# Kernel optimization log

Measured on AMD Instinct MI355X. Metric: run time of the kernel, lower is better.

## Reference

```python
import jax, jax.numpy as jnp
import numpy as np

DIM = 32          # d_model == channel dim of the volume
D_STATE = 16
D_CONV = 4
EXPAND = 2
D_INNER = EXPAND * DIM        # 64
DT_RANK = max(1, (DIM + 15) // 16)  # ceil(d_model/16) = 2
LN_EPS = 1e-5


def setup_inputs() -> dict:
    key = jax.random.key(0)
    ks = jax.random.split(key, 12)
    B, Dd, Hh, Ww = 1, 32, 32, 32
    sc = 0.02
    x = jax.random.normal(ks[0], (B, DIM, Dd, Hh, Ww), jnp.float32)
    ln_w = jnp.ones((DIM,), jnp.float32)
    ln_b = jnp.zeros((DIM,), jnp.float32)
    in_proj_w = jax.random.normal(ks[1], (2 * D_INNER, DIM), jnp.float32) * sc
    conv_w = jax.random.normal(ks[2], (D_INNER, 1, D_CONV), jnp.float32) * sc
    conv_b = jnp.zeros((D_INNER,), jnp.float32)
    x_proj_w = jax.random.normal(ks[3], (DT_RANK + 2 * D_STATE, D_INNER), jnp.float32) * sc
    dt_proj_w = jax.random.normal(ks[4], (D_INNER, DT_RANK), jnp.float32) * sc
    dt_proj_b = jax.random.uniform(ks[5], (D_INNER,), jnp.float32, -4.0, -2.0)  # small softplus(dt) at init
    # Mamba S4D-real init: A = -[1..d_state], stored as A_log
    A_log = jnp.log(jnp.broadcast_to(jnp.arange(1, D_STATE + 1, dtype=jnp.float32), (D_INNER, D_STATE)))
    D_param = jnp.ones((D_INNER,), jnp.float32)
    out_proj_w = jax.random.normal(ks[6], (DIM, D_INNER), jnp.float32) * sc
    return {
        "x": x, "ln_w": ln_w, "ln_b": ln_b, "in_proj_w": in_proj_w,
        "conv_w": conv_w, "conv_b": conv_b, "x_proj_w": x_proj_w,
        "dt_proj_w": dt_proj_w, "dt_proj_b": dt_proj_b, "A_log": A_log,
        "D_param": D_param, "out_proj_w": out_proj_w,
    }


def _mamba_layer(x, ln_w, ln_b, in_proj_w, conv_w, conv_b, x_proj_w,
                 dt_proj_w, dt_proj_b, A_log, D_param, out_proj_w):
    B, C, Dd, Hh, Ww = x.shape
    L = Dd * Hh * Ww
    # z-scan flatten: (B, C, D, H, W) -> (B, L, C)
    xf = x.reshape(B, C, L).transpose(0, 2, 1)
    # LayerNorm over channel dim
    mu = jnp.mean(xf, axis=-1, keepdims=True)
    var = jnp.mean(jnp.square(xf - mu), axis=-1, keepdims=True)
    xn = (xf - mu) * jax.lax.rsqrt(var + LN_EPS) * ln_w + ln_b
    # in_proj -> x, z branches
    xz = xn @ in_proj_w.T                      # (B, L, 2*d_inner)
    x_in, z = jnp.split(xz, 2, axis=-1)
    # depthwise causal conv1d over sequence
    xt = x_in.transpose(0, 2, 1)               # (B, d_inner, L)
    xc = jax.lax.conv_general_dilated(
        xt, conv_w, window_strides=(1,), padding=[(D_CONV - 1, 0)],
        feature_group_count=D_INNER)
    xc = jax.nn.silu(xc + conv_b[None, :, None]).transpose(0, 2, 1)  # (B, L, d_inner)
    # input-dependent dt, B, C
    x_dbl = xc @ x_proj_w.T                    # (B, L, dt_rank + 2*d_state)
    dt, Bm, Cm = jnp.split(x_dbl, [DT_RANK, DT_RANK + D_STATE], axis=-1)
    delta = jax.nn.softplus(dt @ dt_proj_w.T + dt_proj_b)            # (B, L, d_inner)
    A = -jnp.exp(A_log)                        # (d_inner, d_state)
    # discretize: h_t = exp(delta*A) h_{t-1} + delta*B_t*x_t
    dA = jnp.exp(delta[..., None] * A)                               # (B, L, d_inner, d_state)
    dBx = delta[..., None] * Bm[:, :, None, :] * xc[..., None]       # (B, L, d_inner, d_state)
    def comb(e1, e2):
        a1, b1 = e1
        a2, b2 = e2
        return (a1 * a2, a2 * b1 + b2)
    _, h = jax.lax.associative_scan(comb, (dA, dBx), axis=1)         # parallel linear recurrence
    y = jnp.einsum('blds,bls->bld', h, Cm) + xc * D_param            # (B, L, d_inner)
    y = y * jax.nn.silu(z)
    out = y @ out_proj_w.T                     # (B, L, C)
    # unpermute z-scan
    return out.transpose(0, 2, 1).reshape(B, C, Dd, Hh, Ww)


def reference(x, ln_w, ln_b, in_proj_w, conv_w, conv_b, x_proj_w,
              dt_proj_w, dt_proj_b, A_log, D_param, out_proj_w):
    return _mamba_layer(x, ln_w, ln_b, in_proj_w, conv_w, conv_b, x_proj_w,
                        dt_proj_w, dt_proj_b, A_log, D_param, out_proj_w)
```

## Files before the change

kernel.cpp:

```cpp
#include <hip/hip_runtime.h>
#include <hip/hip_bf16.h>

constexpr int L   = 32768;
constexpr int CD  = 32;
constexpr int DI  = 64;
constexpr int DS  = 16;
constexpr int LC  = 32;
constexpr int NCH = L / LC;
constexpr int NPAIR = DI * DS;

constexpr size_t FL        = (size_t)DI * L;
constexpr size_t OFF_XC    = 0;
constexpr size_t OFF_DELTA = FL;
constexpr size_t OFF_BM    = 2 * FL;
constexpr size_t OFF_CM    = OFF_BM + (size_t)DS * L;
constexpr size_t OFF_APROD = OFF_CM + (size_t)DS * L;
constexpr size_t OFF_CARRY = OFF_APROD;
constexpr size_t OFF_BACC  = OFF_APROD + (size_t)NCH * NPAIR;

__device__ __forceinline__ float bf2f(__hip_bfloat16 v) { return __bfloat162float(v); }

__device__ __forceinline__ bool detect_bf16(const void* ln_w) {
    return ((const unsigned short*)ln_w)[0] == 0x3F80;
}
__device__ __forceinline__ float ldin(const void* p, size_t i, bool bf16) {
    return bf16 ? bf2f(((const __hip_bfloat16*)p)[i]) : ((const float*)p)[i];
}

__device__ __forceinline__ float dot32_g(const void* w, int row, const float* xv, bool isb) {
    float acc = 0.f;
    if (isb) {
        const __hip_bfloat16* p = (const __hip_bfloat16*)w + (size_t)row * 32;
        #pragma unroll
        for (int c = 0; c < 32; ++c) acc += bf2f(p[c]) * xv[c];
    } else {
        const float4* p = (const float4*)((const float*)w + (size_t)row * 32);
        #pragma unroll
        for (int q = 0; q < 8; ++q) {
            const float4 w4 = p[q];
            acc += w4.x * xv[4*q] + w4.y * xv[4*q+1] + w4.z * xv[4*q+2] + w4.w * xv[4*q+3];
        }
    }
    return acc;
}

__global__ __launch_bounds__(256, 2) void k12_featurize_scan(
    const void* __restrict__ x,
    const void* __restrict__ ln_w,
    const void* __restrict__ ln_b,
    const void* __restrict__ in_proj_w,
    const void* __restrict__ conv_w,
    const void* __restrict__ conv_b,
    const void* __restrict__ x_proj_w,
    const void* __restrict__ dt_proj_w,
    const void* __restrict__ dt_proj_b,
    const void* __restrict__ A_log,
    float* __restrict__ ws)
{
    __shared__ __align__(16) char smem[33808];
    float (*xin_s)[37]  = (float(*)[37])(smem);
    float (*sxc)[36]    = (float(*)[36])(smem);
    char* AR = smem + 9472;
    float (*xn_s)[33]   = (float(*)[33])(AR);
    float (*w_in_s)[32] = (float(*)[32])(AR + 4624);
    float (*sdl)[36]    = (float(*)[36])(AR);
    float (*sbm)[36]    = (float(*)[36])(AR + 9216);
    char* FW = smem + 22288;
    float (*w_xp)[64]   = (float(*)[64])(FW);
    float (*w_cv)[5]    = (float(*)[5])(FW + 8704);
    float (*w_dt)[3]    = (float(*)[3])(FW + 9984);
    float* b_dt_s = (float*)(FW + 10752);
    float* b_cv_s = (float*)(FW + 11008);
    float* lnw_s  = (float*)(FW + 11264);
    float* lnb_s  = (float*)(FW + 11392);

    const int tid = threadIdx.x;
    const int l0  = blockIdx.x * LC;
    const bool isb = detect_bf16(ln_w);

    if (isb) {
        const __hip_bfloat16* ipw = (const __hip_bfloat16*)in_proj_w;
        const __hip_bfloat16* xpw = (const __hip_bfloat16*)x_proj_w;
        for (int i = tid; i < 64 * 32; i += 256) ((float*)w_in_s)[i] = bf2f(ipw[i]);
        for (int i = tid; i < 34 * 64; i += 256) ((float*)w_xp)[i] = bf2f(xpw[i]);
    } else {
        const float4* ipw = (const float4*)in_proj_w;
        const float4* xpw = (const float4*)x_proj_w;
        #pragma unroll
        for (int k = 0; k < 2; ++k) ((float4*)w_in_s)[tid + 256 * k] = ipw[tid + 256 * k];
        for (int i = tid; i < 544; i += 256) ((float4*)w_xp)[i] = xpw[i];
    }
    w_cv[tid >> 2][tid & 3] = ldin(conv_w, tid, isb);
    if (tid < 128) w_dt[tid >> 1][tid & 1] = ldin(dt_proj_w, tid, isb);
    if (tid < 64) { b_dt_s[tid] = ldin(dt_proj_b, tid, isb); b_cv_s[tid] = ldin(conv_b, tid, isb); }
    if (tid < 32) { lnw_s[tid] = ldin(ln_w, tid, isb); lnb_s[tid] = ldin(ln_b, tid, isb); }
    __syncthreads();

    if (tid < 140) {
        const int pos = tid >> 2;
        const int q   = tid & 3;
        const int l = l0 - 3 + pos;
        const bool valid = (l >= 0);
        const int lc = valid ? l : 0;
        float xq[8];
        #pragma unroll
        for (int i = 0; i < 8; ++i) xq[i] = ldin(x, (size_t)(q * 8 + i) * L + lc, isb);
        float s = 0.f;
        #pragma unroll
        for (int i = 0; i < 8; ++i) s += xq[i];
        s += __shfl_xor(s, 1);
        s += __shfl_xor(s, 2);
        const float mu = s * (1.f / CD);
        float d2 = 0.f;
        #pragma unroll
        for (int i = 0; i < 8; ++i) { const float dc = xq[i] - mu; d2 += dc * dc; }
        d2 += __shfl_xor(d2, 1);
        d2 += __shfl_xor(d2, 2);
        const float rstd = rsqrtf(d2 * (1.f / CD) + 1e-5f);
        #pragma unroll
        for (int i = 0; i < 8; ++i) {
            const int ch = q * 8 + i;
            xn_s[pos][ch] = valid ? ((xq[i] - mu) * rstd * lnw_s[ch] + lnb_s[ch]) : 0.f;
        }
    }
    __syncthreads();

    {
        const int colq = tid & 31;
        const int rgrp = tid >> 5;
        float xv[CD];
        #pragma unroll
        for (int c = 0; c < CD; ++c) xv[c] = xn_s[colq][c];
        #pragma unroll 2
        for (int j = 0; j < 8; ++j) {
            const int row = rgrp * 8 + j;
            const float4* wr = (const float4*)w_in_s[row];
            float a0 = 0.f;
            #pragma unroll
            for (int q = 0; q < 8; ++q) {
                const float4 w4 = wr[q];
                a0 += w4.x * xv[4*q] + w4.y * xv[4*q+1] + w4.z * xv[4*q+2] + w4.w * xv[4*q+3];
            }
            xin_s[row][colq] = a0;
        }
        if (tid < 192) {
            const int row = tid & 63;
            const int cH  = 32 + (tid >> 6);
            float xvh[CD];
            #pragma unroll
            for (int c = 0; c < CD; ++c) xvh[c] = xn_s[cH][c];
            xin_s[row][cH] = dot32_g(in_proj_w, row, xvh, isb);
        }
    }
    __syncthreads();

    {
        const int h  = tid & 7;
        const int pq = tid >> 3;
        const int l  = l0 + pq;
        const int dbase = h * 8;
        float xcv[8];
        #pragma unroll
        for (int i = 0; i < 8; ++i) {
            const int d = dbase + i;
            float acc = b_cv_s[d];
            #pragma unroll
            for (int k = 0; k < 4; ++k) acc += w_cv[d][k] * xin_s[d][pq + k];
            const float v = acc / (1.f + __expf(-acc));
            xcv[i] = v;
            ws[OFF_XC + (size_t)d * L + l] = v;
        }
        float dt0 = 0.f, dt1 = 0.f;
        for (int r = 0; r < 34; ++r) {
            const float4 wa = *(const float4*)&w_xp[r][dbase];
            const float4 wb = *(const float4*)&w_xp[r][dbase + 4];
            float acc = wa.x * xcv[0] + wa.y * xcv[1] + wa.z * xcv[2] + wa.w * xcv[3]
                      + wb.x * xcv[4] + wb.y * xcv[5] + wb.z * xcv[6] + wb.w * xcv[7];
            acc += __shfl_xor(acc, 1);
            acc += __shfl_xor(acc, 2);
            acc += __shfl_xor(acc, 4);
            if (r == 0) dt0 = acc;
            else if (r == 1) dt1 = acc;
            else {
                const int rr = r - 2;
                if (h == (rr >> 2)) {
                    const size_t off = (rr < 16) ? (OFF_BM + (size_t)rr * L)
                                                 : (OFF_CM + (size_t)(rr - 16) * L);
                    ws[off + l] = acc;
                    if (rr < 16) sbm[rr][pq] = acc;
                }
            }
        }
        #pragma unroll
        for (int i = 0; i < 8; ++i) {
            const int d = dbase + i;
            const float tv = dt0 * w_dt[d][0] + dt1 * w_dt[d][1] + b_dt_s[d];
            const float sp = fmaxf(tv, 0.f) + log1pf(__expf(-fabsf(tv)));
            ws[OFF_DELTA + (size_t)d * L + l] = sp;
            sdl[d][pq] = sp;
        }
        __syncthreads();
        #pragma unroll
        for (int i = 0; i < 8; ++i) sxc[dbase + i][pq] = xcv[i];
    }
    __syncthreads();

    {
        const int d = tid >> 2, sg = tid & 3;
        float Aj[4], ap[4] = {1.f, 1.f, 1.f, 1.f}, bb[4] = {0.f, 0.f, 0.f, 0.f};
        #pragma unroll
        for (int j = 0; j < 4; ++j) Aj[j] = -__expf(ldin(A_log, d * DS + sg + 4 * j, isb));

        auto cstep = [&](float dd, float xx, float m0, float m1, float m2, float m3) {
            const float dxc = dd * xx;
            float e;
            e = __expf(dd * Aj[0]); ap[0] *= e; bb[0] = e * bb[0] + dxc * m0;
            e = __expf(dd * Aj[1]); ap[1] *= e; bb[1] = e * bb[1] + dxc * m1;
            e = __expf(dd * Aj[2]); ap[2] *= e; bb[2] = e * bb[2] + dxc * m2;
            e = __expf(dd * Aj[3]); ap[3] *= e; bb[3] = e * bb[3] + dxc * m3;
        };
        for (int t = 0; t < LC; t += 4) {
            const float4 dd4 = *(const float4*)&sdl[d][t];
            const float4 xx4 = *(const float4*)&sxc[d][t];
            const float4 b0 = *(const float4*)&sbm[sg][t];
            const float4 b1 = *(const float4*)&sbm[sg + 4][t];
            const float4 b2 = *(const float4*)&sbm[sg + 8][t];
            const float4 b3 = *(const float4*)&sbm[sg + 12][t];
            cstep(dd4.x, xx4.x, b0.x, b1.x, b2.x, b3.x);
            cstep(dd4.y, xx4.y, b0.y, b1.y, b2.y, b3.y);
            cstep(dd4.z, xx4.z, b0.z, b1.z, b2.z, b3.z);
            cstep(dd4.w, xx4.w, b0.w, b1.w, b2.w, b3.w);
        }
        *(float4*)&ws[OFF_APROD + (size_t)blockIdx.x * NPAIR + tid * 4] = make_float4(ap[0], ap[1], ap[2], ap[3]);
        *(float4*)&ws[OFF_BACC  + (size_t)blockIdx.x * NPAIR + tid * 4] = make_float4(bb[0], bb[1], bb[2], bb[3]);
    }
}

__global__ __launch_bounds__(256) void k3_carry(float* __restrict__ ws)
{
    __shared__ float ctile[4][NCH];
    const int lane = threadIdx.x & 63;
    const int wv   = threadIdx.x >> 6;
    const int bid  = blockIdx.x;
    const int pg   = ((bid & 7) << 5) | (bid >> 3);
    const int p    = pg * 4 + wv;

    float a[16], b[16];
    #pragma unroll
    for (int i = 0; i < 16; ++i) {
        const size_t ch = (size_t)(lane * 16 + i);
        a[i] = ws[OFF_APROD + ch * NPAIR + p];
        b[i] = ws[OFF_BACC  + ch * NPAIR + p];
    }

    float Ag = a[0], Bg = b[0];
    #pragma unroll
    for (int i = 1; i < 16; ++i) { Bg = a[i] * Bg + b[i]; Ag = Ag * a[i]; }
    #pragma unroll
    for (int off = 1; off < 64; off <<= 1) {
        const float pa = __shfl_up(Ag, off);
        const float pb = __shfl_up(Bg, off);
        if (lane >= off) { Bg = Ag * pb + Bg; Ag = Ag * pa; }
    }
    float Pb = __shfl_up(Bg, 1);
    if (lane == 0) Pb = 0.f;
    #pragma unroll
    for (int i = 0; i < 16; ++i) { ctile[wv][lane * 16 + i] = Pb; Pb = a[i] * Pb + b[i]; }
    __syncthreads();
    #pragma unroll
    for (int r = 0; r < 4; ++r) {
        const int ch = threadIdx.x + 256 * r;
        *(float4*)&ws[OFF_CARRY + (size_t)ch * NPAIR + pg * 4] =
            make_float4(ctile[0][ch], ctile[1][ch], ctile[2][ch], ctile[3][ch]);
    }
}

__global__ __launch_bounds__(256, 2) void k45_apply_out(
    const void* __restrict__ x,
    const void* __restrict__ ln_w,
    const void* __restrict__ ln_b,
    const void* __restrict__ in_proj_w,
    const void* __restrict__ A_log,
    const void* __restrict__ D_param,
    const void* __restrict__ out_proj_w,
    float* __restrict__ ws,
    void* __restrict__ out)
{
    __shared__ __align__(16) char smem45[35712];
    float (*sx)[36]      = (float(*)[36])(smem45);
    float (*sy)[36]      = (float(*)[36])(smem45 + 4608);
    float (*sbm)[36]     = (float(*)[36])(smem45 + 13824);
    float (*scm)[36]     = (float(*)[36])(smem45 + 16128);
    float (*w_z)[33]     = (float(*)[33])(smem45 + 18432);
    float (*w_out_s)[65] = (float(*)[65])(smem45 + 26880);
    float* lnw_s = (float*)(smem45 + 35200);
    float* lnb_s = (float*)(smem45 + 35328);
    float* mu_s  = (float*)(smem45 + 35456);
    float* rs_s  = (float*)(smem45 + 35584);

    const int tid = threadIdx.x;
    const int c   = blockIdx.x;
    const size_t t0 = (size_t)c * LC;
    const bool isb = detect_bf16(ln_w);

    {
        const int r = tid >> 3, t4 = (tid & 7) * 4;
        if (isb) {
            const __hip_bfloat16* xb = (const __hip_bfloat16*)x;
            #pragma unroll
            for (int k = 0; k < 4; ++k) sx[r][t4 + k] = bf2f(xb[(size_t)r * L + t0 + t4 + k]);
        } else {
            *(float4*)&sx[r][t4] = *(const float4*)&((const float*)x)[(size_t)r * L + t0 + t4];
        }
    }
    {
        const int q = tid & 127;
        const int r = q >> 3, t4 = (q & 7) * 4;
        const size_t src = ((tid < 128) ? OFF_BM : OFF_CM) + (size_t)r * L + t0 + t4;
        float* dst = (tid < 128) ? &sbm[r][t4] : &scm[r][t4];
        *(float4*)dst = *(const float4*)&ws[src];
    }
    #pragma unroll
    for (int k = 0; k < 8; ++k) {
        const int idx = tid + 256 * k;
        w_z[idx >> 5][idx & 31] = ldin(in_proj_w, (size_t)(64 << 5) + idx, isb);
    }
    #pragma unroll
    for (int k = 0; k < 8; ++k) {
        const int idx = tid + 256 * k;
        w_out_s[idx >> 6][idx & 63] = ldin(out_proj_w, idx, isb);
    }
    if (tid < 32) { lnw_s[tid] = ldin(ln_w, tid, isb); lnb_s[tid] = ldin(ln_b, tid, isb); }
    __syncthreads();

    if (tid < 128) {
        const int pos = tid >> 2;
        const int q   = tid & 3;
        float s = 0.f;
        #pragma unroll
        for (int i = 0; i < 8; ++i) s += sx[q * 8 + i][pos];
        s += __shfl_xor(s, 1);
        s += __shfl_xor(s, 2);
        const float mu = s * (1.f / CD);
        float d2 = 0.f;
        #pragma unroll
        for (int i = 0; i < 8; ++i) { const float dc = sx[q * 8 + i][pos] - mu; d2 += dc * dc; }
        d2 += __shfl_xor(d2, 1);
        d2 += __shfl_xor(d2, 2);
        if (q == 0) { mu_s[pos] = mu; rs_s[pos] = rsqrtf(d2 * (1.f / CD) + 1e-5f); }
    }
    __syncthreads();

    {
        const int pos  = tid & 31;
        const int rgrp = tid >> 5;
        const float mu = mu_s[pos], rstd = rs_s[pos];
        float acc[8] = {0.f, 0.f, 0.f, 0.f, 0.f, 0.f, 0.f, 0.f};
        for (int ch = 0; ch < CD; ++ch) {
            const float xnc = (sx[ch][pos] - mu) * rstd * lnw_s[ch] + lnb_s[ch];
            #pragma unroll
            for (int j = 0; j < 8; ++j) acc[j] += xnc * w_z[rgrp * 8 + j][ch];
        }
        #pragma unroll
        for (int j = 0; j < 8; ++j)
            sy[rgrp * 8 + j][pos] = acc[j] / (1.f + __expf(-acc[j]));
    }
    __syncthreads();

    {
        const int d = tid >> 2, sg = tid & 3;
        float Aj[4];
        #pragma unroll
        for (int j = 0; j < 4; ++j) Aj[j] = -__expf(ldin(A_log, d * DS + sg + 4 * j, isb));
        const float Dd = ldin(D_param, d, isb);
        float hh[4];
        {
            const float4 h4 = *(const float4*)&ws[OFF_CARRY + (size_t)c * NPAIR + tid * 4];
            hh[0] = h4.x; hh[1] = h4.y; hh[2] = h4.z; hh[3] = h4.w;
        }
        const float* dlp = ws + OFF_DELTA + (size_t)d * L + t0;
        const float* xcp = ws + OFF_XC    + (size_t)d * L + t0;

        auto step = [&](float dd, float xx, int col,
                        float m0, float m1, float m2, float m3,
                        float c0, float c1, float c2, float c3) {
            const float dxc = dd * xx;
            float e, ys;
            e = __expf(dd * Aj[0]); hh[0] = e * hh[0] + dxc * m0; ys  = hh[0] * c0;
            e = __expf(dd * Aj[1]); hh[1] = e * hh[1] + dxc * m1; ys += hh[1] * c1;
            e = __expf(dd * Aj[2]); hh[2] = e * hh[2] + dxc * m2; ys += hh[2] * c2;
            e = __expf(dd * Aj[3]); hh[3] = e * hh[3] + dxc * m3; ys += hh[3] * c3;
            ys += __shfl_xor(ys, 1);
            ys += __shfl_xor(ys, 2);
            if (sg == 0) sy[d][col] *= (ys + xx * Dd);
        };
        for (int t = 0; t < LC; t += 4) {
            const float4 dd4 = *(const float4*)(dlp + t);
            const float4 xx4 = *(const float4*)(xcp + t);
            const float4 b0 = *(const float4*)&sbm[sg][t];
            const float4 b1 = *(const float4*)&sbm[sg + 4][t];
            const float4 b2 = *(const float4*)&sbm[sg + 8][t];
            const float4 b3 = *(const float4*)&sbm[sg + 12][t];
            const float4 c0 = *(const float4*)&scm[sg][t];
            const float4 c1 = *(const float4*)&scm[sg + 4][t];
            const float4 c2 = *(const float4*)&scm[sg + 8][t];
            const float4 c3 = *(const float4*)&scm[sg + 12][t];
            step(dd4.x, xx4.x, t,     b0.x, b1.x, b2.x, b3.x, c0.x, c1.x, c2.x, c3.x);
            step(dd4.y, xx4.y, t + 1, b0.y, b1.y, b2.y, b3.y, c0.y, c1.y, c2.y, c3.y);
            step(dd4.z, xx4.z, t + 2, b0.z, b1.z, b2.z, b3.z, c0.z, c1.z, c2.z, c3.z);
            step(dd4.w, xx4.w, t + 3, b0.w, b1.w, b2.w, b3.w, c0.w, c1.w, c2.w, c3.w);
        }
    }
    __syncthreads();

    {
        const int wv   = tid >> 6;
        const int lane = tid & 63;
        const int pos  = lane & 31;
        const int cg   = lane >> 5;
        const int c0   = wv * 8 + cg * 4;
        float acc[4] = {0.f, 0.f, 0.f, 0.f};
        for (int dd = 0; dd < DI; ++dd) {
            const float yv = sy[dd][pos];
            #pragma unroll
            for (int j = 0; j < 4; ++j)
                acc[j] += yv * w_out_s[c0 + j][dd];
        }
        const size_t l = t0 + pos;
        #pragma unroll
        for (int j = 0; j < 4; ++j) {
            const int cc = c0 + j;
            if (isb) ((__hip_bfloat16*)out)[(size_t)cc * L + l] = __float2bfloat16(acc[j]);
            else     ((float*)out)[(size_t)cc * L + l] = acc[j];
        }
    }
}

extern "C" void kernel_launch(void* const* d_in, const int* in_sizes, int n_in,
                              void* d_out, int out_size, void* d_ws, size_t ws_size,
                              hipStream_t stream)
{
    (void)in_sizes; (void)n_in; (void)out_size; (void)ws_size;
    const void* x        = d_in[0];
    const void* ln_w     = d_in[1];
    const void* ln_b     = d_in[2];
    const void* in_pw    = d_in[3];
    const void* conv_w   = d_in[4];
    const void* conv_b   = d_in[5];
    const void* x_pw     = d_in[6];
    const void* dt_pw    = d_in[7];
    const void* dt_pb    = d_in[8];
    const void* A_log    = d_in[9];
    const void* D_param  = d_in[10];
    const void* out_pw   = d_in[11];
    float* ws = (float*)d_ws;

    k12_featurize_scan<<<NCH, 256, 0, stream>>>(x, ln_w, ln_b, in_pw, conv_w, conv_b,
                                                x_pw, dt_pw, dt_pb, A_log, ws);
    k3_carry<<<NPAIR / 4, 256, 0, stream>>>(ws);
    k45_apply_out<<<NCH, 256, 0, stream>>>(x, ln_w, ln_b, in_pw, A_log, D_param,
                                           out_pw, ws, d_out);
}
```

Baseline: 163.1 us.

## Store workspace intermediates in chunk-tiled layout with coalesced float4 writes

Changes the workspace layout for xc, delta, B and C from feature-major over the full sequence to per-chunk contiguous tiles. The featurize kernel now stages C in shared memory as well and writes all tiles with vectorized float4 stores after a barrier, instead of scattered per-element strided stores. The consumer kernel reads the same data as contiguous tiles. This adds a little shared memory and a copy-out phase in exchange for coalesced global traffic.

```diff
diff --git a/kernel.cpp b/kernel.cpp
--- a/kernel.cpp
+++ b/kernel.cpp
@@ -9,12 +9,11 @@
 constexpr int NCH = L / LC;
 constexpr int NPAIR = DI * DS;
 
-constexpr size_t FL        = (size_t)DI * L;
 constexpr size_t OFF_XC    = 0;
-constexpr size_t OFF_DELTA = FL;
-constexpr size_t OFF_BM    = 2 * FL;
-constexpr size_t OFF_CM    = OFF_BM + (size_t)DS * L;
-constexpr size_t OFF_APROD = OFF_CM + (size_t)DS * L;
+constexpr size_t OFF_DELTA = (size_t)NCH * DI * LC;
+constexpr size_t OFF_BM    = 2 * (size_t)NCH * DI * LC;
+constexpr size_t OFF_CM    = OFF_BM + (size_t)NCH * DS * LC;
+constexpr size_t OFF_APROD = OFF_CM + (size_t)NCH * DS * LC;
 constexpr size_t OFF_CARRY = OFF_APROD;
 constexpr size_t OFF_BACC  = OFF_APROD + (size_t)NCH * NPAIR;
 
@@ -57,7 +56,7 @@
     const void* __restrict__ A_log,
     float* __restrict__ ws)
 {
-    __shared__ __align__(16) char smem[33808];
+    __shared__ __align__(16) char smem[34816];
     float (*xin_s)[37]  = (float(*)[37])(smem);
     float (*sxc)[36]    = (float(*)[36])(smem);
     char* AR = smem + 9472;
@@ -65,7 +64,8 @@
     float (*w_in_s)[32] = (float(*)[32])(AR + 4624);
     float (*sdl)[36]    = (float(*)[36])(AR);
     float (*sbm)[36]    = (float(*)[36])(AR + 9216);
-    char* FW = smem + 22288;
+    float (*scm)[36]    = (float(*)[36])(AR + 11520);
+    char* FW = smem + 23296;
     float (*w_xp)[64]   = (float(*)[64])(FW);
     float (*w_cv)[5]    = (float(*)[5])(FW + 8704);
     float (*w_dt)[3]    = (float(*)[3])(FW + 9984);
@@ -157,7 +157,6 @@
     {
         const int h  = tid & 7;
         const int pq = tid >> 3;
-        const int l  = l0 + pq;
         const int dbase = h * 8;
         float xcv[8];
         #pragma unroll
@@ -166,9 +165,7 @@
             float acc = b_cv_s[d];
             #pragma unroll
             for (int k = 0; k < 4; ++k) acc += w_cv[d][k] * xin_s[d][pq + k];
-            const float v = acc / (1.f + __expf(-acc));
-            xcv[i] = v;
-            ws[OFF_XC + (size_t)d * L + l] = v;
+            xcv[i] = acc / (1.f + __expf(-acc));
         }
         float dt0 = 0.f, dt1 = 0.f;
         for (int r = 0; r < 34; ++r) {
@@ -184,10 +181,8 @@
             else {
                 const int rr = r - 2;
                 if (h == (rr >> 2)) {
-                    const size_t off = (rr < 16) ? (OFF_BM + (size_t)rr * L)
-                                                 : (OFF_CM + (size_t)(rr - 16) * L);
-                    ws[off + l] = acc;
                     if (rr < 16) sbm[rr][pq] = acc;
+                    else         scm[rr - 16][pq] = acc;
                 }
             }
         }
@@ -195,15 +190,29 @@
         for (int i = 0; i < 8; ++i) {
             const int d = dbase + i;
             const float tv = dt0 * w_dt[d][0] + dt1 * w_dt[d][1] + b_dt_s[d];
-            const float sp = fmaxf(tv, 0.f) + log1pf(__expf(-fabsf(tv)));
-            ws[OFF_DELTA + (size_t)d * L + l] = sp;
-            sdl[d][pq] = sp;
+            sdl[d][pq] = fmaxf(tv, 0.f) + log1pf(__expf(-fabsf(tv)));
         }
         __syncthreads();
         #pragma unroll
         for (int i = 0; i < 8; ++i) sxc[dbase + i][pq] = xcv[i];
     }
     __syncthreads();
+
+    {
+        const size_t tile = (size_t)blockIdx.x * (DI * LC);
+        #pragma unroll
+        for (int rIt = 0; rIt < 2; ++rIt) {
+            const int j = tid + 256 * rIt;
+            const int dd = j >> 3, k4 = (j & 7) * 4;
+            *(float4*)&ws[OFF_DELTA + tile + dd * LC + k4] = *(const float4*)&sdl[dd][k4];
+            *(float4*)&ws[OFF_XC    + tile + dd * LC + k4] = *(const float4*)&sxc[dd][k4];
+        }
+        const size_t btile = (size_t)blockIdx.x * (DS * LC);
+        const int j = tid & 127;
+        const int rr = j >> 3, k4 = (j & 7) * 4;
+        if (tid < 128) *(float4*)&ws[OFF_BM + btile + rr * LC + k4] = *(const float4*)&sbm[rr][k4];
+        else           *(float4*)&ws[OFF_CM + btile + rr * LC + k4] = *(const float4*)&scm[rr][k4];
+    }
 
     {
         const int d = tid >> 2, sg = tid & 3;
@@ -314,9 +323,10 @@
         }
     }
     {
+        const size_t btile = (size_t)c * (DS * LC);
         const int q = tid & 127;
         const int r = q >> 3, t4 = (q & 7) * 4;
-        const size_t src = ((tid < 128) ? OFF_BM : OFF_CM) + (size_t)r * L + t0 + t4;
+        const size_t src = ((tid < 128) ? OFF_BM : OFF_CM) + btile + r * LC + t4;
         float* dst = (tid < 128) ? &sbm[r][t4] : &scm[r][t4];
         *(float4*)dst = *(const float4*)&ws[src];
     }
@@ -378,8 +388,9 @@
             const float4 h4 = *(const float4*)&ws[OFF_CARRY + (size_t)c * NPAIR + tid * 4];
             hh[0] = h4.x; hh[1] = h4.y; hh[2] = h4.z; hh[3] = h4.w;
         }
-        const float* dlp = ws + OFF_DELTA + (size_t)d * L + t0;
-        const float* xcp = ws + OFF_XC    + (size_t)d * L + t0;
+        const size_t tile = (size_t)c * (DI * LC);
+        const float* dlp = ws + OFF_DELTA + tile + d * LC;
+        const float* xcp = ws + OFF_XC    + tile + d * LC;
 
         auto step = [&](float dd, float xx, int col,
                         float m0, float m1, float m2, float m3,
```

New measurement: 163.2 us. Within noise of the previous version (+0.0%).
